# Kernel optimization log

Hardware: AMD Instinct MI355X
Metric: run time of the kernel (lower is better)

## Reference

```python
import jax, jax.numpy as jnp
import numpy as np

B, A, OBS, NACT, H, D = 8192, 8, 128, 32, 256, 64  # batch, n_agents, obs_shape, n_actions, rnn_hidden_dim, attn_dim
N = B * A


def setup_inputs() -> dict:
    key = jax.random.key(0)
    ks = jax.random.split(key, 12)
    s = 0.02
    return {
        "o": jax.random.normal(ks[0], (N, OBS), dtype=jnp.float32),
        "o_next": jax.random.normal(ks[1], (N, OBS), dtype=jnp.float32),
        "h": jax.random.normal(ks[2], (N, H), dtype=jnp.float32),
        "actions": jax.random.uniform(ks[3], (N, A, NACT), dtype=jnp.float32),
        "wq_w": jax.random.normal(ks[4], (D, 2 * OBS), dtype=jnp.float32) * s,
        "wq_b": jnp.zeros((D,), dtype=jnp.float32),
        "wk_w": jax.random.normal(ks[5], (D, NACT), dtype=jnp.float32) * s,
        "wk_b": jnp.zeros((D,), dtype=jnp.float32),
        "wv1_w": jax.random.normal(ks[6], (D, H + NACT), dtype=jnp.float32) * s,
        "wv1_b": jnp.zeros((D,), dtype=jnp.float32),
        "wv2_w": jax.random.normal(ks[7], (NACT, D), dtype=jnp.float32) * s,
        "wv2_b": jnp.zeros((NACT,), dtype=jnp.float32),
    }


def reference(o, o_next, h, actions, wq_w, wq_b, wk_w, wk_b, wv1_w, wv1_b, wv2_w, wv2_b):
    n, a, nact = actions.shape           # [N, A, n_actions]
    d = wq_w.shape[0]                    # attn_dim
    hdim = h.shape[-1]
    b = n // a
    # query: [N, D]
    query = jnp.concatenate([o, o_next], axis=-1) @ wq_w.T + wq_b
    # key: [N, A, D]
    key = (actions.reshape(-1, nact) @ wk_w.T + wk_b).reshape(n, a, d)
    # value: repeat h per attended agent -> [B*A*A, H]
    h_rep = jnp.tile(h.reshape(b, a, hdim), (1, a, 1)).reshape(-1, hdim)
    inps_v = jnp.concatenate([h_rep, actions.reshape(-1, nact)], axis=-1)
    hid = jax.nn.relu(inps_v @ wv1_w.T + wv1_b)
    value = (hid @ wv2_w.T + wv2_b).reshape(n, a, nact)
    # attention scores with self-masked diagonal
    scale = 1.0 / (float(d) ** 0.5)
    scores = jnp.einsum('nd,nad->na', query * scale, key).reshape(b, a, a)
    eye = jnp.eye(a, dtype=bool)
    scores = jnp.where(eye[None, :, :], jnp.asarray(-1e9, scores.dtype), scores)
    attn = jax.nn.softmax(scores, axis=-1).reshape(n, a, 1)
    q = jnp.sum(value * attn, axis=1)    # [N, n_actions]
    return q
```

## Files before the change

### kernel.cpp

```cpp
#include <hip/hip_runtime.h>
#include <hip/hip_bf16.h>

typedef __attribute__((ext_vector_type(8))) short bf16x8;
typedef __attribute__((ext_vector_type(4))) float f32x4;

#define MFMA(A, B, C) __builtin_amdgcn_mfma_f32_16x16x32_bf16((A), (B), (C), 0, 0, 0)

#define OFF_TB    0
#define OFF_WT_H  128
#define OFF_WT_L  16512
#define OFF_WHV_H 32896
#define OFF_WHV_L 65664
#define OFF_WA_H  98432
#define OFF_WA_L  102528

#define SM_HV   0
#define SM_AT   4352
#define SM_SS   4864
#define SM_TOT  7168

__device__ __forceinline__ unsigned short f2bf(float v) {
    unsigned u = __builtin_bit_cast(unsigned, v);
    return (unsigned short)((u + 0x7fffu + ((u >> 16) & 1u)) >> 16);
}
__device__ __forceinline__ float bf2f(unsigned short b) {
    return __builtin_bit_cast(float, ((unsigned)b) << 16);
}
__device__ __forceinline__ ushort2 splitf(float v) {
    unsigned short h = f2bf(v);
    unsigned short l = f2bf(v - bf2f(h));
    return make_ushort2(h, l);
}

__device__ __forceinline__ unsigned as_u32(__hip_bfloat162 v) {
    unsigned u;
    __builtin_memcpy(&u, &v, sizeof(u));
    return u;
}

__device__ __forceinline__ void split2(float x, float y, unsigned& h, unsigned& l) {
    __hip_bfloat162 h2 = __float22bfloat162_rn(make_float2(x, y));
    float2 hf = __bfloat1622float2(h2);
    __hip_bfloat162 l2 = __float22bfloat162_rn(make_float2(x - hf.x, y - hf.y));
    h = as_u32(h2);
    l = as_u32(l2);
}
__device__ __forceinline__ void split8(float4 a, float4 b, bf16x8& hi, bf16x8& lo) {
    uint4 H, L;
    split2(a.x, a.y, H.x, L.x);
    split2(a.z, a.w, H.y, L.y);
    split2(b.x, b.y, H.z, L.z);
    split2(b.z, b.w, H.w, L.w);
    hi = __builtin_bit_cast(bf16x8, H);
    lo = __builtin_bit_cast(bf16x8, L);
}
__device__ __forceinline__ unsigned pk2(float x, float y) {
    return as_u32(__float22bfloat162_rn(make_float2(x, y)));
}

__global__ __launch_bounds__(256) void k_setup(const float* __restrict__ wq_w,
                                               const float* __restrict__ wq_b,
                                               const float* __restrict__ wk_w,
                                               const float* __restrict__ wv1,
                                               char* __restrict__ ws) {
    int gid = blockIdx.x * 256 + threadIdx.x;
    if (gid < 8192) {
        int k = gid >> 8, c = gid & 255;
        float acc = 0.f;
#pragma unroll 8
        for (int d = 0; d < 64; ++d) acc = fmaf(wk_w[d * 32 + k], wq_w[d * 256 + c], acc);
        ushort2 s = splitf(0.125f * acc);
        ((unsigned short*)(ws + OFF_WT_H))[gid] = s.x;
        ((unsigned short*)(ws + OFF_WT_L))[gid] = s.y;
    } else if (gid < 24576) {
        int i = gid - 8192;
        ushort2 s = splitf(wv1[(i >> 8) * 288 + (i & 255)]);
        ((unsigned short*)(ws + OFF_WHV_H))[i] = s.x;
        ((unsigned short*)(ws + OFF_WHV_L))[i] = s.y;
    } else if (gid < 26624) {
        int i = gid - 24576;
        ushort2 s = splitf(wv1[(i >> 5) * 288 + 256 + (i & 31)]);
        ((unsigned short*)(ws + OFF_WA_H))[i] = s.x;
        ((unsigned short*)(ws + OFF_WA_L))[i] = s.y;
    } else if (gid < 26656) {
        int k = gid - 26624;
        float b = 0.f;
#pragma unroll 8
        for (int d = 0; d < 64; ++d) b = fmaf(wk_w[d * 32 + k], wq_b[d], b);
        ((float*)(ws + OFF_TB))[k] = 0.125f * b;
    }
}

__global__ __launch_bounds__(64, 4) void fused(
    const float* __restrict__ o, const float* __restrict__ onx,
    const float* __restrict__ h, const float* __restrict__ act,
    const float* __restrict__ wv1b, const float* __restrict__ wv2,
    const float* __restrict__ wv2b, const char* __restrict__ ws,
    float* __restrict__ out)
{
    __shared__ __align__(16) char sm[SM_TOT];
    float* HV = (float*)(sm + SM_HV);
    float* AT = (float*)(sm + SM_AT);
    unsigned short* SS = (unsigned short*)(sm + SM_SS);

    const int lane = threadIdx.x;
    const int l15  = lane & 15;
    const int quad = lane >> 4;
    const int n0   = blockIdx.x * 16;
    const int myrow = n0 + l15;

    const f32x4 zv = {0.f, 0.f, 0.f, 0.f};
    f32x4 acc_hv[4] = {zv, zv, zv, zv};
    f32x4 acc_t[2]  = {zv, zv};

    float4 xa[8], xb[8];
#pragma unroll
    for (int ch = 0; ch < 8; ++ch) {
        const float* src = (ch < 4)
            ? o   + (size_t)myrow * 128 + ch * 32 + quad * 8
            : onx + (size_t)myrow * 128 + (ch - 4) * 32 + quad * 8;
        xa[ch] = ((const float4*)src)[0];
        xb[ch] = ((const float4*)src)[1];
    }
#pragma unroll
    for (int ch = 0; ch < 8; ++ch) {
        bf16x8 Bh, Bl;
        split8(xa[ch], xb[ch], Bh, Bl);
#pragma unroll
        for (int mt = 0; mt < 2; ++mt) {
            int off = ((mt * 16 + l15) * 256 + ch * 32 + quad * 8) * 2;
            bf16x8 Ah = *(const bf16x8*)(ws + OFF_WT_H + off);
            bf16x8 Al = *(const bf16x8*)(ws + OFF_WT_L + off);
            acc_t[mt] = MFMA(Ah, Bh, acc_t[mt]);
            acc_t[mt] = MFMA(Ah, Bl, acc_t[mt]);
            acc_t[mt] = MFMA(Al, Bh, acc_t[mt]);
        }
    }
#pragma unroll
    for (int ch = 0; ch < 8; ++ch) {
        const float* src = h + (size_t)myrow * 256 + ch * 32 + quad * 8;
        xa[ch] = ((const float4*)src)[0];
        xb[ch] = ((const float4*)src)[1];
    }
#pragma unroll
    for (int ch = 0; ch < 8; ++ch) {
        bf16x8 Bh, Bl;
        split8(xa[ch], xb[ch], Bh, Bl);
#pragma unroll
        for (int mt = 0; mt < 4; ++mt) {
            int off = ((mt * 16 + l15) * 256 + ch * 32 + quad * 8) * 2;
            bf16x8 Ah = *(const bf16x8*)(ws + OFF_WHV_H + off);
            bf16x8 Al = *(const bf16x8*)(ws + OFF_WHV_L + off);
            acc_hv[mt] = MFMA(Ah, Bh, acc_hv[mt]);
            acc_hv[mt] = MFMA(Ah, Bl, acc_hv[mt]);
            acc_hv[mt] = MFMA(Al, Bh, acc_hv[mt]);
        }
    }

    const float* arow = act + (size_t)myrow * 256;
    float4 av0[8], av1[8];
#pragma unroll
    for (int j = 0; j < 8; ++j) {
        av0[j] = *(const float4*)(arow + j * 32 + quad * 4);
        av1[j] = *(const float4*)(arow + j * 32 + 16 + quad * 4);
    }

#pragma unroll
    for (int mt = 0; mt < 4; ++mt) {
        int d0 = mt * 16 + quad * 4;
        float4 b = *(const float4*)&wv1b[d0];
        f32x4 a = acc_hv[mt];
        *(float4*)&HV[l15 * 68 + d0] =
            make_float4(a[0] + b.x, a[1] + b.y, a[2] + b.z, a[3] + b.w);
    }

    {
        float t8[8];
        const float* tb = (const float*)(ws + OFF_TB);
#pragma unroll
        for (int mt = 0; mt < 2; ++mt) {
            float4 b = *(const float4*)&tb[mt * 16 + quad * 4];
            t8[mt * 4 + 0] = acc_t[mt][0] + b.x;
            t8[mt * 4 + 1] = acc_t[mt][1] + b.y;
            t8[mt * 4 + 2] = acc_t[mt][2] + b.z;
            t8[mt * 4 + 3] = acc_t[mt][3] + b.w;
        }
        float sc[8];
#pragma unroll
        for (int j = 0; j < 8; ++j) {
            float s = 0.f;
            s = fmaf(t8[0], av0[j].x, s);
            s = fmaf(t8[1], av0[j].y, s);
            s = fmaf(t8[2], av0[j].z, s);
            s = fmaf(t8[3], av0[j].w, s);
            s = fmaf(t8[4], av1[j].x, s);
            s = fmaf(t8[5], av1[j].y, s);
            s = fmaf(t8[6], av1[j].z, s);
            s = fmaf(t8[7], av1[j].w, s);
            sc[j] = s;
        }
#pragma unroll
        for (int j = 0; j < 8; ++j) {
            sc[j] += __shfl_xor(sc[j], 16);
            sc[j] += __shfl_xor(sc[j], 32);
        }
        const int diag = l15 & 7;
        float mx = -1e30f;
#pragma unroll
        for (int j = 0; j < 8; ++j) if (j != diag) mx = fmaxf(mx, sc[j]);
        float ex[8], sum = 0.f;
#pragma unroll
        for (int j = 0; j < 8; ++j) {
            ex[j] = (j == diag) ? 0.f : __expf(sc[j] - mx);
            sum += ex[j];
        }
        float inv = 1.f / sum;
        if (quad == 0) {
            *(float4*)&AT[l15 * 8] =
                make_float4(ex[0] * inv, ex[1] * inv, ex[2] * inv, ex[3] * inv);
            *(float4*)&AT[l15 * 8 + 4] =
                make_float4(ex[4] * inv, ex[5] * inv, ex[6] * inv, ex[7] * inv);
        }
    }

    bf16x8 WAh[4], WAl[4];
#pragma unroll
    for (int mt = 0; mt < 4; ++mt) {
        int off = ((mt * 16 + l15) * 32 + quad * 8) * 2;
        WAh[mt] = *(const bf16x8*)(ws + OFF_WA_H + off);
        WAl[mt] = *(const bf16x8*)(ws + OFF_WA_L + off);
    }
    __syncthreads();

    const int jB  = l15 & 7;
    const int nbh = l15 >> 3;
#pragma unroll
    for (int half = 0; half < 2; ++half) {
        float4 bv0[4], bv1[4];
#pragma unroll
        for (int ii = 0; ii < 4; ++ii) {
            int nb = (half * 4 + ii) * 2 + nbh;
            const float* ap = act + (size_t)(n0 + nb) * 256 + jB * 32 + quad * 8;
            bv0[ii] = ((const float4*)ap)[0];
            bv1[ii] = ((const float4*)ap)[1];
        }
#pragma unroll
        for (int ii = 0; ii < 4; ++ii) {
            int nt = half * 4 + ii;
            int nb = nt * 2 + nbh;
            bf16x8 Bh, Bl;
            split8(bv0[ii], bv1[ii], Bh, Bl);
            f32x4 accB[4] = {zv, zv, zv, zv};
#pragma unroll
            for (int mt = 0; mt < 4; ++mt) {
                accB[mt] = MFMA(WAh[mt], Bh, accB[mt]);
                accB[mt] = MFMA(WAh[mt], Bl, accB[mt]);
                accB[mt] = MFMA(WAl[mt], Bh, accB[mt]);
            }
            int hrow = (nb & 8) + jB;
            float at = AT[nb * 8 + jB];
#pragma unroll
            for (int mt = 0; mt < 4; ++mt) {
                int d0 = mt * 16 + quad * 4;
                float4 hv4 = *(const float4*)&HV[hrow * 68 + d0];
                float r0 = at * fmaxf(accB[mt][0] + hv4.x, 0.f);
                float r1 = at * fmaxf(accB[mt][1] + hv4.y, 0.f);
                float r2 = at * fmaxf(accB[mt][2] + hv4.z, 0.f);
                float r3 = at * fmaxf(accB[mt][3] + hv4.w, 0.f);
#pragma unroll
                for (int m = 1; m <= 4; m <<= 1) {
                    r0 += __shfl_xor(r0, m);
                    r1 += __shfl_xor(r1, m);
                    r2 += __shfl_xor(r2, m);
                    r3 += __shfl_xor(r3, m);
                }
                if (jB == 0)
                    *(uint2*)&SS[nb * 72 + d0] = make_uint2(pk2(r0, r1), pk2(r2, r3));
            }
        }
    }

    float4 wva[4], wvb[4];
#pragma unroll
    for (int c = 0; c < 4; ++c) {
        const float* wp = wv2 + ((c >> 1) * 16 + l15) * 64 + (c & 1) * 32 + quad * 8;
        wva[c] = ((const float4*)wp)[0];
        wvb[c] = ((const float4*)wp)[1];
    }
    __syncthreads();

    {
        bf16x8 Sb[2];
#pragma unroll
        for (int kc = 0; kc < 2; ++kc)
            Sb[kc] = *(const bf16x8*)&SS[l15 * 72 + kc * 32 + quad * 8];
        f32x4 acc2[2] = {zv, zv};
#pragma unroll
        for (int c = 0; c < 4; ++c) {
            bf16x8 Ah, Al;
            split8(wva[c], wvb[c], Ah, Al);
            acc2[c >> 1] = MFMA(Ah, Sb[c & 1], acc2[c >> 1]);
            acc2[c >> 1] = MFMA(Al, Sb[c & 1], acc2[c >> 1]);
        }
#pragma unroll
        for (int et = 0; et < 2; ++et) {
            int e0 = et * 16 + quad * 4;
            float4 b = *(const float4*)&wv2b[e0];
            f32x4 a = acc2[et];
            *(float4*)&out[(size_t)(n0 + l15) * 32 + e0] =
                make_float4(a[0] + b.x, a[1] + b.y, a[2] + b.z, a[3] + b.w);
        }
    }
}

extern "C" void kernel_launch(void* const* d_in, const int* in_sizes, int n_in,
                              void* d_out, int out_size, void* d_ws, size_t ws_size,
                              hipStream_t stream) {
    const float* o     = (const float*)d_in[0];
    const float* onx   = (const float*)d_in[1];
    const float* h     = (const float*)d_in[2];
    const float* act   = (const float*)d_in[3];
    const float* wq_w  = (const float*)d_in[4];
    const float* wq_b  = (const float*)d_in[5];
    const float* wk_w  = (const float*)d_in[6];
    const float* wv1_w = (const float*)d_in[8];
    const float* wv1_b = (const float*)d_in[9];
    const float* wv2_w = (const float*)d_in[10];
    const float* wv2_b = (const float*)d_in[11];
    float* out = (float*)d_out;
    char* ws   = (char*)d_ws;

    k_setup<<<105, 256, 0, stream>>>(wq_w, wq_b, wk_w, wv1_w, ws);
    fused<<<4096, 64, 0, stream>>>(o, onx, h, act, wv1_b, wv2_w, wv2_b, ws, out);
}
```

Baseline: 251.3 us.

## Split each 16-row block across two waves handling eight rows each

```diff
diff --git a/kernel.cpp b/kernel.cpp
--- a/kernel.cpp
+++ b/kernel.cpp
@@ -91,7 +91,7 @@
     }
 }
 
-__global__ __launch_bounds__(64, 4) void fused(
+__global__ __launch_bounds__(128, 8) void fused(
     const float* __restrict__ o, const float* __restrict__ onx,
     const float* __restrict__ h, const float* __restrict__ act,
     const float* __restrict__ wv1b, const float* __restrict__ wv2,
@@ -99,15 +99,19 @@
     float* __restrict__ out)
 {
     __shared__ __align__(16) char sm[SM_TOT];
-    float* HV = (float*)(sm + SM_HV);
-    float* AT = (float*)(sm + SM_AT);
-    unsigned short* SS = (unsigned short*)(sm + SM_SS);
-
-    const int lane = threadIdx.x;
+
+    const int tid  = threadIdx.x;
+    const int wid  = tid >> 6;
+    const int lane = tid & 63;
     const int l15  = lane & 15;
     const int quad = lane >> 4;
-    const int n0   = blockIdx.x * 16;
-    const int myrow = n0 + l15;
+    const int r8   = l15 & 7;
+    const int n0   = blockIdx.x * 16 + wid * 8;
+    const int myrow = n0 + r8;
+
+    float* HV = (float*)(sm + SM_HV) + wid * 544;
+    float* AT = (float*)(sm + SM_AT) + wid * 64;
+    unsigned short* SS = (unsigned short*)(sm + SM_SS) + wid * 576;
 
     const f32x4 zv = {0.f, 0.f, 0.f, 0.f};
     f32x4 acc_hv[4] = {zv, zv, zv, zv};
@@ -165,13 +169,15 @@
         av1[j] = *(const float4*)(arow + j * 32 + 16 + quad * 4);
     }
 
-#pragma unroll
-    for (int mt = 0; mt < 4; ++mt) {
-        int d0 = mt * 16 + quad * 4;
-        float4 b = *(const float4*)&wv1b[d0];
-        f32x4 a = acc_hv[mt];
-        *(float4*)&HV[l15 * 68 + d0] =
-            make_float4(a[0] + b.x, a[1] + b.y, a[2] + b.z, a[3] + b.w);
+    if (l15 < 8) {
+#pragma unroll
+        for (int mt = 0; mt < 4; ++mt) {
+            int d0 = mt * 16 + quad * 4;
+            float4 b = *(const float4*)&wv1b[d0];
+            f32x4 a = acc_hv[mt];
+            *(float4*)&HV[r8 * 68 + d0] =
+                make_float4(a[0] + b.x, a[1] + b.y, a[2] + b.z, a[3] + b.w);
+        }
     }
 
     {
@@ -204,7 +210,7 @@
             sc[j] += __shfl_xor(sc[j], 16);
             sc[j] += __shfl_xor(sc[j], 32);
         }
-        const int diag = l15 & 7;
+        const int diag = r8;
         float mx = -1e30f;
 #pragma unroll
         for (int j = 0; j < 8; ++j) if (j != diag) mx = fmaxf(mx, sc[j]);
@@ -215,10 +221,10 @@
             sum += ex[j];
         }
         float inv = 1.f / sum;
-        if (quad == 0) {
-            *(float4*)&AT[l15 * 8] =
+        if (lane < 8) {
+            *(float4*)&AT[lane * 8] =
                 make_float4(ex[0] * inv, ex[1] * inv, ex[2] * inv, ex[3] * inv);
-            *(float4*)&AT[l15 * 8 + 4] =
+            *(float4*)&AT[lane * 8 + 4] =
                 make_float4(ex[4] * inv, ex[5] * inv, ex[6] * inv, ex[7] * inv);
         }
     }
@@ -234,20 +240,18 @@
 
     const int jB  = l15 & 7;
     const int nbh = l15 >> 3;
-#pragma unroll
-    for (int half = 0; half < 2; ++half) {
+    {
         float4 bv0[4], bv1[4];
 #pragma unroll
         for (int ii = 0; ii < 4; ++ii) {
-            int nb = (half * 4 + ii) * 2 + nbh;
+            int nb = ii * 2 + nbh;
             const float* ap = act + (size_t)(n0 + nb) * 256 + jB * 32 + quad * 8;
             bv0[ii] = ((const float4*)ap)[0];
             bv1[ii] = ((const float4*)ap)[1];
         }
 #pragma unroll
         for (int ii = 0; ii < 4; ++ii) {
-            int nt = half * 4 + ii;
-            int nb = nt * 2 + nbh;
+            int nb = ii * 2 + nbh;
             bf16x8 Bh, Bl;
             split8(bv0[ii], bv1[ii], Bh, Bl);
             f32x4 accB[4] = {zv, zv, zv, zv};
@@ -257,12 +261,11 @@
                 accB[mt] = MFMA(WAh[mt], Bl, accB[mt]);
                 accB[mt] = MFMA(WAl[mt], Bh, accB[mt]);
             }
-            int hrow = (nb & 8) + jB;
             float at = AT[nb * 8 + jB];
 #pragma unroll
             for (int mt = 0; mt < 4; ++mt) {
                 int d0 = mt * 16 + quad * 4;
-                float4 hv4 = *(const float4*)&HV[hrow * 68 + d0];
+                float4 hv4 = *(const float4*)&HV[jB * 68 + d0];
                 float r0 = at * fmaxf(accB[mt][0] + hv4.x, 0.f);
                 float r1 = at * fmaxf(accB[mt][1] + hv4.y, 0.f);
                 float r2 = at * fmaxf(accB[mt][2] + hv4.z, 0.f);
@@ -293,7 +296,7 @@
         bf16x8 Sb[2];
 #pragma unroll
         for (int kc = 0; kc < 2; ++kc)
-            Sb[kc] = *(const bf16x8*)&SS[l15 * 72 + kc * 32 + quad * 8];
+            Sb[kc] = *(const bf16x8*)&SS[r8 * 72 + kc * 32 + quad * 8];
         f32x4 acc2[2] = {zv, zv};
 #pragma unroll
         for (int c = 0; c < 4; ++c) {
@@ -302,13 +305,15 @@
             acc2[c >> 1] = MFMA(Ah, Sb[c & 1], acc2[c >> 1]);
             acc2[c >> 1] = MFMA(Al, Sb[c & 1], acc2[c >> 1]);
         }
-#pragma unroll
-        for (int et = 0; et < 2; ++et) {
-            int e0 = et * 16 + quad * 4;
-            float4 b = *(const float4*)&wv2b[e0];
-            f32x4 a = acc2[et];
-            *(float4*)&out[(size_t)(n0 + l15) * 32 + e0] =
-                make_float4(a[0] + b.x, a[1] + b.y, a[2] + b.z, a[3] + b.w);
+        if (l15 < 8) {
+#pragma unroll
+            for (int et = 0; et < 2; ++et) {
+                int e0 = et * 16 + quad * 4;
+                float4 b = *(const float4*)&wv2b[e0];
+                f32x4 a = acc2[et];
+                *(float4*)&out[(size_t)(n0 + r8) * 32 + e0] =
+                    make_float4(a[0] + b.x, a[1] + b.y, a[2] + b.z, a[3] + b.w);
+            }
         }
     }
 }
@@ -331,5 +336,5 @@
     char* ws   = (char*)d_ws;
 
     k_setup<<<105, 256, 0, stream>>>(wq_w, wq_b, wk_w, wv1_w, ws);
-    fused<<<4096, 64, 0, stream>>>(o, onx, h, act, wv1_b, wv2_w, wv2_b, ws, out);
-}
+    fused<<<4096, 128, 0, stream>>>(o, onx, h, act, wv1_b, wv2_w, wv2_b, ws, out);
+}
```

After: 383.2 us. 1.53x slower.
